# Kernel tuning notes

Hardware: AMD Instinct MI355X
Metric: run time of the kernel (lower is better)

Reference implementation:

```python
import jax, jax.numpy as jnp
import numpy as np

# init constants (match init_kwargs)
NGH, SUB_Q, SUB_D, POS_D, NEG_D, BORDER, SUB_D_NEG = 7, 8, 1, 2, 4, 16, 8
BATCH_STRIDE = 512.0  # hardcoded `b * 512` offset in the original cdist call


def _offsets():
    # faithful port of NghSampler.precompute_offsets
    rad = (NGH // SUB_D) * NGH
    pos, neg = [], []
    for j in range(-rad, rad + 1, SUB_D):
        for i in range(-rad, rad + 1, SUB_D):
            d2 = i * i + j * j
            if d2 <= POS_D ** 2:
                pos.append((i, j))
            elif NEG_D ** 2 <= d2 <= NGH ** 2:
                neg.append((i, j))
    return np.array(pos, np.int32).T, np.array(neg, np.int32).T  # [2,P],[2,Nn]


def _grid(step, B, H, W):
    # gen_grid with step > 0: regular grid inside the border, flattened
    xs = np.arange(BORDER, W - BORDER, step)
    ys = np.arange(BORDER, H - BORDER, step)
    H1, W1 = len(ys), len(xs)
    b = np.repeat(np.arange(B), H1 * W1)
    y = np.tile(np.repeat(ys, W1), B)
    x = np.tile(np.tile(xs, H1), B)
    return b, y, x, (B, H1, W1)


def setup_inputs() -> dict:
    key = jax.random.key(0)
    B, D, H, W = 2, 128, 512, 512
    k1, k2, k3, k4, k5 = jax.random.split(key, 5)
    pos_off, neg_off = _offsets()
    return {
        "feat1": jax.random.normal(k1, (B, D, H, W), jnp.float32),
        "feat2": jax.random.normal(k2, (B, D, H, W), jnp.float32),
        "conf1": jax.random.uniform(k3, (B, 1, H, W), jnp.float32),
        "conf2": jax.random.uniform(k4, (B, 1, H, W), jnp.float32),
        # dense flow: target (x, y) coords in image 2, a few out of bounds
        "aflow": jax.random.uniform(k5, (B, 2, H, W), jnp.float32, -10.0, W + 10.0),
        "pos_offsets": jnp.asarray(pos_off),
        "neg_offsets": jnp.asarray(neg_off),
    }


def reference(feat1, feat2, conf1, conf2, aflow, pos_offsets, neg_offsets):
    B, two, H, W = aflow.shape
    b1, y1, x1, shape = _grid(SUB_Q, B, H, W)      # n = B*H1*W1 query points

    f1 = feat1[b1, :, y1, x1]                      # [n, D]
    qconf = conf1[b1, 0, y1, x1].reshape(shape)    # (B, H1, W1)

    # (aflow + 0.5).long(): truncation toward zero, as torch .long()
    xy2 = jnp.transpose(aflow[b1, :, y1, x1] + 0.5).astype(jnp.int32)  # [2, n]
    mask = ((xy2[0] >= 0) & (xy2[1] >= 0) & (xy2[0] < W) & (xy2[1] < H)).reshape(shape)

    def clamp(xy):
        return jnp.stack([jnp.clip(xy[0], 0, W - 1), jnp.clip(xy[1], 0, H - 1)])

    # positive ring: gather feat2 at offset pixels -> [P, n, D], dot with f1
    xy2p = clamp(xy2[:, None, :] + pos_offsets[:, :, None])  # [2, P, n]
    pscores = jnp.einsum('nk,pnk->np', f1, feat2[b1, :, xy2p[1], xy2p[0]])
    # negative ring -> [Nn, n, D]
    xy2n = clamp(xy2[:, None, :] + neg_offsets[:, :, None])  # [2, Nn, n]
    nscores = jnp.einsum('nk,ink->ni', f1, feat2[b1, :, xy2n[1], xy2n[0]])

    # distractors: regular grid over image 2
    b3, y3, x3, _ = _grid(SUB_D_NEG, B, H, W)      # n3 points
    d3 = feat2[b3, :, y3, x3]                      # [n3, D]
    dscores = jnp.einsum('nk,ik->ni', f1, d3)      # [n, n3]

    # cdist with per-batch 512 offset (un-clamped xy2, as in the original)
    qx = xy2[0].astype(jnp.float32) + BATCH_STRIDE * b1
    qy = xy2[1].astype(jnp.float32) + BATCH_STRIDE * b1
    dx = x3.astype(np.float32) + BATCH_STRIDE * b3
    dy = y3.astype(np.float32) + BATCH_STRIDE * b3
    dis = jnp.sqrt((qx[:, None] - dx[None, :]) ** 2 + (qy[:, None] - dy[None, :]) ** 2)
    dscores = jnp.where(dis < NEG_D, 0.0, dscores)

    scores = jnp.concatenate([pscores, nscores, dscores], axis=1)
    n, P = pscores.shape
    gt = jnp.concatenate([jnp.ones((n, P), jnp.uint8),
                          jnp.zeros((n, scores.shape[1] - P), jnp.uint8)], axis=1)
    return scores, gt, mask, qconf
```

## Files before the change

kernel.cpp:

```cpp
#include <hip/hip_runtime.h>
#include <hip/hip_bf16.h>
#include <stdint.h>

#define B_ 2
#define D_ 128
#define H_ 512
#define W_ 512
#define G_ 60
#define NQ_ 7200
#define BORDER_ 16
#define STEP_ 8

typedef __attribute__((ext_vector_type(8))) short short8;
typedef __attribute__((ext_vector_type(4))) float f32x4;
typedef __attribute__((ext_vector_type(4))) uint32_t u32x4;

__device__ __forceinline__ float bf_lo(uint32_t u){ return __builtin_bit_cast(float, u << 16); }
__device__ __forceinline__ float bf_hi(uint32_t u){ return __builtin_bit_cast(float, u & 0xffff0000u); }

__device__ __forceinline__ uint32_t pack2bf(float lo, float hi){
  uint16_t l = __builtin_bit_cast(uint16_t, __float2bfloat16(lo));
  uint16_t h = __builtin_bit_cast(uint16_t, __float2bfloat16(hi));
  return (uint32_t)l | ((uint32_t)h << 16);
}

__global__ __launch_bounds__(256) void gtzero_k(f32x4* __restrict__ gt, size_t n4){
  size_t i = (size_t)blockIdx.x * 256 + threadIdx.x;
  size_t stride = (size_t)gridDim.x * 256;
  f32x4 z = {0.f, 0.f, 0.f, 0.f};
  for (; i < n4; i += stride)
    __builtin_nontemporal_store(z, gt + i);
}

__global__ __launch_bounds__(256) void transpose_k(const float* __restrict__ src,
                                                   __hip_bfloat16* __restrict__ dst){
  __shared__ uint32_t lds2[64][65];
  int b = blockIdx.z, y = blockIdx.y, x0 = blockIdx.x * 64;
  int tid = threadIdx.x;
  size_t plane = (size_t)H_ * W_;

  int xq = tid & 15;
  int eg = tid >> 4;
  size_t base_in = (((size_t)b * D_) * H_ + y) * W_ + x0 + 4 * xq;
  #pragma unroll
  for (int it = 0; it < 4; ++it){
    int e = eg + 16 * it;
    f32x4 lo = __builtin_nontemporal_load(
        reinterpret_cast<const f32x4*>(src + base_in + (size_t)(2 * e) * plane));
    f32x4 hi = __builtin_nontemporal_load(
        reinterpret_cast<const f32x4*>(src + base_in + (size_t)(2 * e + 1) * plane));
    lds2[e][4 * xq + 0] = pack2bf(lo[0], hi[0]);
    lds2[e][4 * xq + 1] = pack2bf(lo[1], hi[1]);
    lds2[e][4 * xq + 2] = pack2bf(lo[2], hi[2]);
    lds2[e][4 * xq + 3] = pack2bf(lo[3], hi[3]);
  }
  __syncthreads();

  int eq = tid & 15;
  int xb = tid >> 4;
  size_t pixbase = (((size_t)b * H_ + y) * W_ + x0);
  #pragma unroll
  for (int it = 0; it < 4; ++it){
    int x = xb + 16 * it;
    u32x4 v;
    v[0] = lds2[4 * eq + 0][x];
    v[1] = lds2[4 * eq + 1][x];
    v[2] = lds2[4 * eq + 2][x];
    v[3] = lds2[4 * eq + 3][x];
    *reinterpret_cast<u32x4*>(dst + (pixbase + x) * D_ + 8 * eq) = v;
  }
}

template<bool USE_T>
__global__ __launch_bounds__(128) void prep_k(
    const float* __restrict__ feat1, const float* __restrict__ feat2,
    const __hip_bfloat16* __restrict__ f2t,
    const float* __restrict__ conf1, const float* __restrict__ aflow,
    __hip_bfloat16* __restrict__ f1o, __hip_bfloat16* __restrict__ d3o,
    float2* __restrict__ qxy, float2* __restrict__ dxy,
    float* __restrict__ omask, float* __restrict__ oqconf)
{
  int n = blockIdx.x;
  int b = n / (G_ * G_); int r = n % (G_ * G_);
  int iy = r / G_, ix = r % G_;
  int y1 = BORDER_ + iy * STEP_, x1 = BORDER_ + ix * STEP_;
  int tid = threadIdx.x;
  size_t pix = ((size_t)b * H_ + y1) * W_ + x1;
  if (tid < 64){
    int d = tid * 2;
    size_t o = (((size_t)b * D_ + d) * H_ + y1) * W_ + x1;
    float lo = feat1[o];
    float hi = feat1[o + (size_t)H_ * W_];
    *reinterpret_cast<uint32_t*>(f1o + (size_t)n * D_ + d) = pack2bf(lo, hi);
    if (tid == 0){
      float ax = aflow[(((size_t)b * 2 + 0) * H_ + y1) * W_ + x1];
      float ay = aflow[(((size_t)b * 2 + 1) * H_ + y1) * W_ + x1];
      int x2 = (int)(ax + 0.5f);
      int y2 = (int)(ay + 0.5f);
      omask[n] = (x2 >= 0 && y2 >= 0 && x2 < W_ && y2 < H_) ? 1.0f : 0.0f;
      oqconf[n] = conf1[pix];
      float bs = 512.0f * (float)b;
      qxy[n] = make_float2((float)x2 + bs, (float)y2 + bs);
      dxy[n] = make_float2((float)x1 + bs, (float)y1 + bs);
    }
  } else {
    int d = (tid - 64) * 2;
    uint32_t u;
    if (USE_T){
      u = *reinterpret_cast<const uint32_t*>(f2t + pix * D_ + d);
    } else {
      size_t o = (((size_t)b * D_ + d) * H_ + y1) * W_ + x1;
      u = pack2bf(feat2[o], feat2[o + (size_t)H_ * W_]);
    }
    *reinterpret_cast<uint32_t*>(d3o + (size_t)n * D_ + d) = u;
  }
}

template<bool USE_T>
__global__ __launch_bounds__(256) void posneg_k(
    const __hip_bfloat16* __restrict__ f1o,
    const __hip_bfloat16* __restrict__ f2t,
    const float* __restrict__ feat2,
    const float* __restrict__ aflow,
    const int* __restrict__ pos, const int* __restrict__ neg,
    int P, int NN, float* __restrict__ out, int NCOL, size_t GTOFF)
{
  int n = blockIdx.x;
  int b = n / (G_ * G_); int r = n % (G_ * G_);
  int iy = r / G_, ix = r % G_;
  int y1 = BORDER_ + iy * STEP_, x1 = BORDER_ + ix * STEP_;
  int tid = threadIdx.x;
  int l16 = tid & 15, grp = tid >> 4;

  const uint4 av = *reinterpret_cast<const uint4*>(f1o + (size_t)n * D_ + l16 * 8);
  float a[8];
  a[0] = bf_lo(av.x); a[1] = bf_hi(av.x); a[2] = bf_lo(av.y); a[3] = bf_hi(av.y);
  a[4] = bf_lo(av.z); a[5] = bf_hi(av.z); a[6] = bf_lo(av.w); a[7] = bf_hi(av.w);

  float ax = aflow[(((size_t)b * 2 + 0) * H_ + y1) * W_ + x1];
  float ay = aflow[(((size_t)b * 2 + 1) * H_ + y1) * W_ + x1];
  int x2 = (int)(ax + 0.5f), y2 = (int)(ay + 0.5f);

  int NP = P + NN;
  for (int p0 = 0; p0 < NP; p0 += 16){
    int p = p0 + grp;
    float s = 0.0f;
    if (p < NP){
      int ox, oy;
      if (p < P){ ox = pos[p]; oy = pos[P + p]; }
      else      { ox = neg[p - P]; oy = neg[NN + p - P]; }
      int px = min(max(x2 + ox, 0), W_ - 1);
      int py = min(max(y2 + oy, 0), H_ - 1);
      if (USE_T){
        const uint4 v = *reinterpret_cast<const uint4*>(
            f2t + (((size_t)b * H_ + py) * W_ + px) * D_ + l16 * 8);
        s = a[0]*bf_lo(v.x) + a[1]*bf_hi(v.x) + a[2]*bf_lo(v.y) + a[3]*bf_hi(v.y)
          + a[4]*bf_lo(v.z) + a[5]*bf_hi(v.z) + a[6]*bf_lo(v.w) + a[7]*bf_hi(v.w);
      } else {
        size_t o = (((size_t)b * D_ + l16 * 8) * H_ + py) * W_ + px;
        #pragma unroll
        for (int j = 0; j < 8; ++j) s += a[j] * feat2[o + (size_t)j * H_ * W_];
      }
    }
    s += __shfl_xor(s, 1); s += __shfl_xor(s, 2);
    s += __shfl_xor(s, 4); s += __shfl_xor(s, 8);
    if (p < NP && l16 == 0){
      size_t idx = (size_t)n * NCOL + p;
      out[idx] = s;
      out[GTOFF + idx] = (p < P) ? 1.0f : 0.0f;
    }
  }
}

__global__ __launch_bounds__(256) void gemm_k(
    const __hip_bfloat16* __restrict__ f1o, const __hip_bfloat16* __restrict__ d3o,
    const float2* __restrict__ qxy, const float2* __restrict__ dxy,
    float* __restrict__ out, int NCOL, int CB)
{
  __shared__ float sT[4][16][100];
  int m0 = blockIdx.x * 16;
  int tid = threadIdx.x;
  int lane = tid & 63, wid = tid >> 6;
  int r16 = lane & 15, kg = lane >> 4;

  short8 af[4];
  #pragma unroll
  for (int ks = 0; ks < 4; ++ks)
    af[ks] = *reinterpret_cast<const short8*>(
        f1o + (size_t)(m0 + r16) * D_ + ks * 32 + kg * 8);

  #pragma unroll 1
  for (int it = 0; it < 4; ++it){
    int c = blockIdx.y * 16 + wid * 4 + it;
    int cn0 = c * 64;
    int nc = (c == 111) ? 96 : 64;

    f32x4 acc[6] = {};
    #pragma unroll
    for (int j = 0; j < 6; ++j){
      if (j * 16 < nc){
        int nn = cn0 + j * 16 + r16;
        #pragma unroll
        for (int ks = 0; ks < 4; ++ks){
          short8 br = *reinterpret_cast<const short8*>(
              d3o + (size_t)nn * D_ + ks * 32 + kg * 8);
          acc[j] = __builtin_amdgcn_mfma_f32_16x16x32_bf16(br, af[ks], acc[j], 0, 0, 0);
        }
      }
    }

    #pragma unroll
    for (int j = 0; j < 6; ++j)
      if (j * 16 < nc)
        *reinterpret_cast<f32x4*>(&sT[wid][r16][j * 16 + kg * 4]) = acc[j];

    float2 dcA = dxy[cn0 + lane];
    float2 dcB = dxy[cn0 + ((nc > 64) ? 64 + (lane & 31) : lane)];

    size_t S = (size_t)m0 * NCOL + CB + cn0;
    #pragma unroll
    for (int r = 0; r < 16; ++r, S += NCOL){
      float2 q = qxy[m0 + r];
      float v = sT[wid][r][lane];
      float ddx = q.x - dcA.x, ddy = q.y - dcA.y;
      float val = (ddx * ddx + ddy * ddy < 16.0f) ? 0.0f : v;
      __builtin_nontemporal_store(val, out + S + lane);
      if (nc > 64 && lane < 32){
        float v2 = sT[wid][r][64 + lane];
        float ddx2 = q.x - dcB.x, ddy2 = q.y - dcB.y;
        float val2 = (ddx2 * ddx2 + ddy2 * ddy2 < 16.0f) ? 0.0f : v2;
        __builtin_nontemporal_store(val2, out + S + 64 + lane);
      }
    }
  }
}

extern "C" void kernel_launch(void* const* d_in, const int* in_sizes, int n_in,
                              void* d_out, int out_size, void* d_ws, size_t ws_size,
                              hipStream_t stream)
{
  const float* feat1 = (const float*)d_in[0];
  const float* feat2 = (const float*)d_in[1];
  const float* conf1 = (const float*)d_in[2];
  const float* aflow = (const float*)d_in[4];
  const int* pos = (const int*)d_in[5];
  const int* neg = (const int*)d_in[6];
  int P = in_sizes[5] / 2, NN = in_sizes[6] / 2;
  int NCOL = P + NN + NQ_;
  size_t GTOFF = (size_t)NQ_ * (size_t)NCOL;
  float* out = (float*)d_out;

  char* ws = (char*)d_ws;
  __hip_bfloat16* f1o = (__hip_bfloat16*)ws;
  __hip_bfloat16* d3o = (__hip_bfloat16*)(ws + 1843200);
  float2* qxy = (float2*)(ws + 3686400);
  float2* dxy = (float2*)(ws + 3744000);
  __hip_bfloat16* f2t = (__hip_bfloat16*)(ws + 3801600);
  size_t needT = 3801600ull + (size_t)B_ * H_ * W_ * D_ * 2;
  bool useT = ws_size >= needT;

  float* omask  = out + 2 * GTOFF;
  float* oqconf = omask + NQ_;

  gtzero_k<<<2048, 256, 0, stream>>>((f32x4*)(out + GTOFF), GTOFF / 4);

  if (useT){
    transpose_k<<<dim3(W_ / 64, H_, B_), 256, 0, stream>>>(feat2, f2t);
    prep_k<true><<<NQ_, 128, 0, stream>>>(feat1, feat2, f2t, conf1, aflow,
                                          f1o, d3o, qxy, dxy, omask, oqconf);
    gemm_k<<<dim3(NQ_ / 16, 7), 256, 0, stream>>>(f1o, d3o, qxy, dxy,
                                                  out, NCOL, P + NN);
    posneg_k<true><<<NQ_, 256, 0, stream>>>(f1o, f2t, feat2, aflow, pos, neg,
                                            P, NN, out, NCOL, GTOFF);
  } else {
    prep_k<false><<<NQ_, 128, 0, stream>>>(feat1, feat2, f2t, conf1, aflow,
                                           f1o, d3o, qxy, dxy, omask, oqconf);
    gemm_k<<<dim3(NQ_ / 16, 7), 256, 0, stream>>>(f1o, d3o, qxy, dxy,
                                                  out, NCOL, P + NN);
    posneg_k<false><<<NQ_, 256, 0, stream>>>(f1o, f2t, feat2, aflow, pos, neg,
                                             P, NN, out, NCOL, GTOFF);
  }
}
```

Before: 290.9 us.

## Double-buffer distractor tile loads to overlap with output drain in gemm_k

After: 289.2 us. No clear change (-0.6%).

```diff
diff --git a/kernel.cpp b/kernel.cpp
--- a/kernel.cpp
+++ b/kernel.cpp
@@ -182,6 +182,7 @@
   int tid = threadIdx.x;
   int lane = tid & 63, wid = tid >> 6;
   int r16 = lane & 15, kg = lane >> 4;
+  int cbase = blockIdx.y * 16 + wid * 4;
 
   short8 af[4];
   #pragma unroll
@@ -189,34 +190,40 @@
     af[ks] = *reinterpret_cast<const short8*>(
         f1o + (size_t)(m0 + r16) * D_ + ks * 32 + kg * 8);
 
-  #pragma unroll 1
-  for (int it = 0; it < 4; ++it){
-    int c = blockIdx.y * 16 + wid * 4 + it;
+  short8 bufA[6][4], bufB[6][4];
+
+  auto load_chunk = [&](short8 (&bn)[6][4], int c){
+    int cn0 = c * 64;
+    int nj = (c == 111) ? 6 : 4;
+    #pragma unroll
+    for (int j = 0; j < 6; ++j)
+      if (j < nj){
+        int nn = cn0 + j * 16 + r16;
+        #pragma unroll
+        for (int ks = 0; ks < 4; ++ks)
+          bn[j][ks] = *reinterpret_cast<const short8*>(
+              d3o + (size_t)nn * D_ + ks * 32 + kg * 8);
+      }
+  };
+
+  auto compute_stage = [&](short8 (&bn)[6][4], int c){
+    int nj = (c == 111) ? 6 : 4;
+    #pragma unroll
+    for (int j = 0; j < 6; ++j)
+      if (j < nj){
+        f32x4 acc = {0.f, 0.f, 0.f, 0.f};
+        #pragma unroll
+        for (int ks = 0; ks < 4; ++ks)
+          acc = __builtin_amdgcn_mfma_f32_16x16x32_bf16(bn[j][ks], af[ks], acc, 0, 0, 0);
+        *reinterpret_cast<f32x4*>(&sT[wid][r16][j * 16 + kg * 4]) = acc;
+      }
+  };
+
+  auto drain = [&](int c){
     int cn0 = c * 64;
     int nc = (c == 111) ? 96 : 64;
-
-    f32x4 acc[6] = {};
-    #pragma unroll
-    for (int j = 0; j < 6; ++j){
-      if (j * 16 < nc){
-        int nn = cn0 + j * 16 + r16;
-        #pragma unroll
-        for (int ks = 0; ks < 4; ++ks){
-          short8 br = *reinterpret_cast<const short8*>(
-              d3o + (size_t)nn * D_ + ks * 32 + kg * 8);
-          acc[j] = __builtin_amdgcn_mfma_f32_16x16x32_bf16(br, af[ks], acc[j], 0, 0, 0);
-        }
-      }
-    }
-
-    #pragma unroll
-    for (int j = 0; j < 6; ++j)
-      if (j * 16 < nc)
-        *reinterpret_cast<f32x4*>(&sT[wid][r16][j * 16 + kg * 4]) = acc[j];
-
     float2 dcA = dxy[cn0 + lane];
     float2 dcB = dxy[cn0 + ((nc > 64) ? 64 + (lane & 31) : lane)];
-
     size_t S = (size_t)m0 * NCOL + CB + cn0;
     #pragma unroll
     for (int r = 0; r < 16; ++r, S += NCOL){
@@ -232,7 +239,20 @@
         __builtin_nontemporal_store(val2, out + S + 64 + lane);
       }
     }
-  }
+  };
+
+  load_chunk(bufA, cbase + 0);
+  compute_stage(bufA, cbase + 0);
+  load_chunk(bufB, cbase + 1);
+  drain(cbase + 0);
+  compute_stage(bufB, cbase + 1);
+  load_chunk(bufA, cbase + 2);
+  drain(cbase + 1);
+  compute_stage(bufA, cbase + 2);
+  load_chunk(bufB, cbase + 3);
+  drain(cbase + 2);
+  compute_stage(bufB, cbase + 3);
+  drain(cbase + 3);
 }
 
 extern "C" void kernel_launch(void* const* d_in, const int* in_sizes, int n_in,
```
